# Performance work log

Measured on AMD Instinct MI355X. Metric: run time of the kernel, lower is better.

Reference implementation:

```python
import jax, jax.numpy as jnp
import numpy as np

NL, DM, DS, DC, EX = 4, 1024, 16, 4, 2
DI = EX * DM          # 2048 inner dim
DTR = DM // 16        # 64 dt_rank
HID, OUT = 2048, 1000
B, L = 2, 1024
EPS = 1e-5

def _ln(x, w, b):
    m = jnp.mean(x, -1, keepdims=True)
    v = jnp.var(x, -1, keepdims=True)
    return (x - m) / jnp.sqrt(v + EPS) * w + b

def _silu(x):
    return x * jax.nn.sigmoid(x)

def _dwconv(x, w, b):
    # x: (B,L,C), w: (C,K) depthwise causal conv
    K = w.shape[1]
    xp = jnp.pad(x, ((0, 0), (K - 1, 0), (0, 0)))
    kern = jnp.transpose(w)[:, None, :]  # (K,1,C)
    y = jax.lax.conv_general_dilated(xp, kern, (1,), 'VALID',
                                     dimension_numbers=('NLC', 'LIO', 'NLC'),
                                     feature_group_count=x.shape[-1])
    return y + b

def _selective_scan(xs_, dt, Bm, Cm, A, Dv):
    # xs_, dt: (B,L,DI); Bm, Cm: (B,L,DS); A: (DI,DS); Dv: (DI,)
    def step(h, inp):
        x_t, dt_t, B_t, C_t = inp  # (B,DI),(B,DI),(B,DS),(B,DS)
        dA = jnp.exp(dt_t[..., None] * A)                       # (B,DI,DS)
        h = dA * h + dt_t[..., None] * B_t[:, None, :] * x_t[..., None]
        return h, jnp.einsum('bdn,bn->bd', h, C_t)
    h0 = jnp.zeros((xs_.shape[0], A.shape[0], A.shape[1]), xs_.dtype)
    seq = tuple(jnp.swapaxes(t, 0, 1) for t in (xs_, dt, Bm, Cm))
    _, ys = jax.lax.scan(step, h0, seq)
    return jnp.swapaxes(ys, 0, 1) + xs_ * Dv

def _mamba_block(x, ipw, cw, cb, xpw, dpw, dpb, Alog, Dv, opw):
    xz = jnp.einsum('bld,ed->ble', x, ipw)          # (B,L,2*DI)
    xs_, z = jnp.split(xz, 2, -1)
    xs_ = _silu(_dwconv(xs_, cw, cb))
    xdbl = jnp.einsum('bld,ed->ble', xs_, xpw)      # (B,L,DTR+2*DS)
    dt, Bm, Cm = jnp.split(xdbl, [DTR, DTR + DS], -1)
    dt = jax.nn.softplus(jnp.einsum('blr,dr->bld', dt, dpw) + dpb)
    A = -jnp.exp(Alog)
    y = _selective_scan(xs_, dt, Bm, Cm, A, Dv)
    y = y * _silu(z)
    return jnp.einsum('bld,ed->ble', y, opw)

def setup_inputs() -> dict:
    key = jax.random.key(0)
    ks = jax.random.split(key, 16)
    s = 0.02
    return {
        'x': jax.random.normal(ks[0], (B, L, DM), jnp.float32),
        'ln_w': jnp.ones((NL, DM)), 'ln_b': jnp.zeros((NL, DM)),
        'in_proj_w': jax.random.normal(ks[1], (NL, 2 * DI, DM)) * s,
        'conv_w': jax.random.normal(ks[2], (NL, DI, DC)) * s,
        'conv_b': jnp.zeros((NL, DI)),
        'x_proj_w': jax.random.normal(ks[3], (NL, DTR + 2 * DS, DI)) * s,
        'dt_proj_w': jax.random.normal(ks[4], (NL, DI, DTR)) * s,
        'dt_proj_b': jax.random.uniform(ks[5], (NL, DI), minval=-4.0, maxval=-2.0),
        'A_log': jnp.log(jnp.broadcast_to(jnp.arange(1, DS + 1, dtype=jnp.float32), (NL, DI, DS)) + 0.0),
        'Dv': jnp.ones((NL, DI)),
        'out_proj_w': jax.random.normal(ks[6], (NL, DM, DI)) * s,
        'fn_w': jnp.ones((DM,)), 'fn_b': jnp.zeros((DM,)),
        'h1_w': jax.random.normal(ks[7], (HID, DM)) * s, 'h1_b': jnp.zeros((HID,)),
        'hln_w': jnp.ones((HID,)), 'hln_b': jnp.zeros((HID,)),
        'h2_w': jax.random.normal(ks[8], (OUT, HID)) * s, 'h2_b': jnp.zeros((OUT,)),
    }

def reference(x, ln_w, ln_b, in_proj_w, conv_w, conv_b, x_proj_w, dt_proj_w,
              dt_proj_b, A_log, Dv, out_proj_w, fn_w, fn_b,
              h1_w, h1_b, hln_w, hln_b, h2_w, h2_b):
    for i in range(NL):
        res = x
        xn = _ln(x, ln_w[i], ln_b[i])
        x = _mamba_block(xn, in_proj_w[i], conv_w[i], conv_b[i], x_proj_w[i],
                         dt_proj_w[i], dt_proj_b[i], A_log[i], Dv[i], out_proj_w[i]) + res
    x = _ln(x, fn_w, fn_b)
    last = x[:, -1, :]                               # (B, DM)
    h = jax.nn.gelu(_ln(last @ h1_w.T + h1_b, hln_w, hln_b), approximate=False)
    return h @ h2_w.T + h2_b                         # (B, OUT)
```

## Files before the change

### kernel.cpp

```cpp
#include <hip/hip_runtime.h>

typedef unsigned short u16;
using short8 = __attribute__((ext_vector_type(8))) short;
using f32x4  = __attribute__((ext_vector_type(4))) float;

#define NLAYER 4
#define DMODEL 1024
#define DSTATE 16
#define DINNER 2048
#define DTRANK 64
#define SEQL   1024
#define NBATCH 2
#define MTOK   2048
#define NCH    64
#define CLEN   16

__device__ __forceinline__ u16 f2bf(float f) {
  union { float f; unsigned int u; } cv; cv.f = f;
  return (u16)((cv.u + 0x7FFFu + ((cv.u >> 16) & 1u)) >> 16);
}
__device__ __forceinline__ float bf2f(u16 v) {
  union { unsigned int u; float f; } cv; cv.u = ((unsigned int)v) << 16; return cv.f;
}

__global__ __launch_bounds__(256) void f32_to_bf16_l(const float* __restrict__ src,
                                                     u16* __restrict__ dst, int nper) {
  int l = blockIdx.y;
  int i4 = (blockIdx.x * 256 + threadIdx.x) * 4;
  if (i4 >= nper) return;
  float4 v = *(const float4*)&src[(size_t)l * nper + i4];
  ushort4 o; o.x = f2bf(v.x); o.y = f2bf(v.y); o.z = f2bf(v.z); o.w = f2bf(v.w);
  *(ushort4*)&dst[(size_t)l * nper + i4] = o;
}

__global__ __launch_bounds__(256) void cvt_pad_xproj_l(const float* __restrict__ src,
                                                       u16* __restrict__ dst) {
  int l = blockIdx.y;
  int i4 = (blockIdx.x * 256 + threadIdx.x) * 4;
  int row = i4 >> 11, col = i4 & 2047;
  float4 v = make_float4(0.f, 0.f, 0.f, 0.f);
  if (row < 96) v = *(const float4*)&src[(size_t)l * 96 * 2048 + row * 2048 + col];
  ushort4 o; o.x = f2bf(v.x); o.y = f2bf(v.y); o.z = f2bf(v.z); o.w = f2bf(v.w);
  *(ushort4*)&dst[(size_t)l * 128 * 2048 + i4] = o;
}

__global__ __launch_bounds__(256) void ln_to_bf16_k(const float* __restrict__ X,
    const float* __restrict__ w, const float* __restrict__ b, u16* __restrict__ out) {
  int row = blockIdx.x, tid = threadIdx.x;
  const float* x = X + (size_t)row * 1024;
  float4 v = ((const float4*)x)[tid];
  float s = v.x + v.y + v.z + v.w;
  float q = v.x*v.x + v.y*v.y + v.z*v.z + v.w*v.w;
  for (int o = 32; o; o >>= 1) { s += __shfl_down(s, o); q += __shfl_down(q, o); }
  __shared__ float sb[4], qb[4];
  int wv = tid >> 6, lane = tid & 63;
  if (lane == 0) { sb[wv] = s; qb[wv] = q; }
  __syncthreads();
  s = sb[0] + sb[1] + sb[2] + sb[3];
  q = qb[0] + qb[1] + qb[2] + qb[3];
  float mean = s * (1.f / 1024.f);
  float var  = q * (1.f / 1024.f) - mean * mean;
  float rstd = rsqrtf(var + 1e-5f);
  float4 wv4 = ((const float4*)w)[tid];
  float4 bv4 = ((const float4*)b)[tid];
  ushort4 o4;
  o4.x = f2bf((v.x - mean) * rstd * wv4.x + bv4.x);
  o4.y = f2bf((v.y - mean) * rstd * wv4.y + bv4.y);
  o4.z = f2bf((v.z - mean) * rstd * wv4.z + bv4.z);
  o4.w = f2bf((v.w - mean) * rstd * wv4.w + bv4.w);
  ((ushort4*)(out + (size_t)row * 1024))[tid] = o4;
}

__device__ __forceinline__ void stage_tile(const u16* G, int ld, int row0, int k0,
                                           u16* S, int tid) {
  int w = tid >> 6;
#pragma unroll
  for (int j = 0; j < 2; ++j) {
    int t = tid + j * 256;
    int r = t >> 2;
    int c = (t & 3) << 3;
    const u16* g = G + (size_t)(row0 + r) * ld + (k0 + c);
    u16* s = S + w * 512 + j * 2048;
    __builtin_amdgcn_global_load_lds((const __attribute__((address_space(1))) void*)g,
                                     (__attribute__((address_space(3))) void*)s,
                                     16, 0, 0);
  }
}

template<int EPI>
__global__ __launch_bounds__(256) void gemm_bt(const u16* __restrict__ A,
    const u16* __restrict__ Bw, float* __restrict__ C,
    int lda, int ldb, int ldc, int kchunk) {
  __shared__ u16 As[2][128 * 32];
  __shared__ u16 Bs[2][128 * 32];
  int tid = threadIdx.x;
  int bm = blockIdx.x, bn = blockIdx.y;
  int kb = blockIdx.z * kchunk, ke = kb + kchunk;
  int lane = tid & 63, w = tid >> 6;
  int wr = (w >> 1) * 64, wc = (w & 1) * 64;
  int fr = lane & 15;
  int kg = (lane >> 4) * 8;
  f32x4 acc[4][4] = {};
  int cur = 0;
  stage_tile(A, lda, bm * 128, kb, As[0], tid);
  stage_tile(Bw, ldb, bn * 128, kb, Bs[0], tid);
  __syncthreads();
  for (int k0 = kb; k0 < ke; k0 += 32) {
    int kn = k0 + 32;
    if (kn < ke) {
      stage_tile(A, lda, bm * 128, kn, As[cur ^ 1], tid);
      stage_tile(Bw, ldb, bn * 128, kn, Bs[cur ^ 1], tid);
    }
    short8 a[4], b[4];
#pragma unroll
    for (int mf = 0; mf < 4; ++mf)
      a[mf] = *(const short8*)&As[cur][(wr + mf * 16 + fr) * 32 + kg];
#pragma unroll
    for (int nf = 0; nf < 4; ++nf)
      b[nf] = *(const short8*)&Bs[cur][(wc + nf * 16 + fr) * 32 + kg];
#pragma unroll
    for (int mf = 0; mf < 4; ++mf)
#pragma unroll
      for (int nf = 0; nf < 4; ++nf)
        acc[mf][nf] = __builtin_amdgcn_mfma_f32_16x16x32_bf16(a[mf], b[nf], acc[mf][nf], 0, 0, 0);
    __syncthreads();
    cur ^= 1;
  }
  int r0 = bm * 128 + wr + (lane >> 4) * 4;
  int c0 = bn * 128 + wc + fr;
#pragma unroll
  for (int mf = 0; mf < 4; ++mf) {
#pragma unroll
    for (int nf = 0; nf < 4; ++nf) {
#pragma unroll
      for (int r = 0; r < 4; ++r) {
        int gr = r0 + mf * 16 + r;
        int gc = c0 + nf * 16;
        float v = acc[mf][nf][r];
        size_t idx = (size_t)gr * ldc + gc;
        if (EPI == 1) {
          ((u16*)C)[idx] = f2bf(v);
        } else {
          atomicAdd(&C[idx], v);
        }
      }
    }
  }
}

__global__ __launch_bounds__(256) void conv_silu_k(const u16* __restrict__ xzb,
    const float* __restrict__ cw, const float* __restrict__ cb,
    u16* __restrict__ xsb) {
  int idx = blockIdx.x * 256 + threadIdx.x;
  int m = idx >> 9;
  int d = (idx & 511) << 2;
  int t = m & (SEQL - 1);
  float4 w0 = *(const float4*)&cw[(d + 0) * 4];
  float4 w1 = *(const float4*)&cw[(d + 1) * 4];
  float4 w2 = *(const float4*)&cw[(d + 2) * 4];
  float4 w3 = *(const float4*)&cw[(d + 3) * 4];
  float4 acc = *(const float4*)&cb[d];
#pragma unroll
  for (int j = 0; j < 4; ++j) {
    int tt = t - 3 + j;
    if (tt >= 0) {
      ushort4 xv = *(const ushort4*)&xzb[(size_t)(m - 3 + j) * 4096 + d];
      acc.x += bf2f(xv.x) * ((const float*)&w0)[j];
      acc.y += bf2f(xv.y) * ((const float*)&w1)[j];
      acc.z += bf2f(xv.z) * ((const float*)&w2)[j];
      acc.w += bf2f(xv.w) * ((const float*)&w3)[j];
    }
  }
  float4 o;
  o.x = acc.x / (1.f + __expf(-acc.x));
  o.y = acc.y / (1.f + __expf(-acc.y));
  o.z = acc.z / (1.f + __expf(-acc.z));
  o.w = acc.w / (1.f + __expf(-acc.w));
  ushort4 ob; ob.x = f2bf(o.x); ob.y = f2bf(o.y); ob.z = f2bf(o.z); ob.w = f2bf(o.w);
  *(ushort4*)&xsb[(size_t)m * 2048 + d] = ob;
}

__global__ __launch_bounds__(256) void gemm_dt_k(const float* __restrict__ Af,
    const u16* __restrict__ Bw, const float* __restrict__ bias, u16* __restrict__ Cout) {
  __shared__ u16 As[128 * 32];
  __shared__ u16 Bs[128 * 32];
  int tid = threadIdx.x;
  int bm = blockIdx.x, bn = blockIdx.y;
  int lane = tid & 63, w = tid >> 6;
  int wr = (w >> 1) * 64, wc = (w & 1) * 64;
  int fr = lane & 15;
  int kg = (lane >> 4) * 8;
  f32x4 acc[4][4] = {};
  int r  = tid >> 1;
  int cc = (tid & 1) * 16;
  for (int k0 = 0; k0 < 64; k0 += 32) {
    const float* src = &Af[(size_t)(bm * 128 + r) * 128 + k0 + cc];
    float4 f0 = *(const float4*)&src[0];
    float4 f1 = *(const float4*)&src[4];
    float4 f2 = *(const float4*)&src[8];
    float4 f3 = *(const float4*)&src[12];
    short8 o0, o1;
    o0[0]=(short)f2bf(f0.x); o0[1]=(short)f2bf(f0.y); o0[2]=(short)f2bf(f0.z); o0[3]=(short)f2bf(f0.w);
    o0[4]=(short)f2bf(f1.x); o0[5]=(short)f2bf(f1.y); o0[6]=(short)f2bf(f1.z); o0[7]=(short)f2bf(f1.w);
    o1[0]=(short)f2bf(f2.x); o1[1]=(short)f2bf(f2.y); o1[2]=(short)f2bf(f2.z); o1[3]=(short)f2bf(f2.w);
    o1[4]=(short)f2bf(f3.x); o1[5]=(short)f2bf(f3.y); o1[6]=(short)f2bf(f3.z); o1[7]=(short)f2bf(f3.w);
    __syncthreads();
    *(short8*)&As[r * 32 + cc]     = o0;
    *(short8*)&As[r * 32 + cc + 8] = o1;
    stage_tile(Bw, 64, bn * 128, k0, Bs, tid);
    __syncthreads();
    short8 a[4], b[4];
#pragma unroll
    for (int mf = 0; mf < 4; ++mf)
      a[mf] = *(const short8*)&As[(wr + mf * 16 + fr) * 32 + kg];
#pragma unroll
    for (int nf = 0; nf < 4; ++nf)
      b[nf] = *(const short8*)&Bs[(wc + nf * 16 + fr) * 32 + kg];
#pragma unroll
    for (int mf = 0; mf < 4; ++mf)
#pragma unroll
      for (int nf = 0; nf < 4; ++nf)
        acc[mf][nf] = __builtin_amdgcn_mfma_f32_16x16x32_bf16(a[mf], b[nf], acc[mf][nf], 0, 0, 0);
  }
  int r0 = bm * 128 + wr + (lane >> 4) * 4;
  int c0 = bn * 128 + wc + fr;
#pragma unroll
  for (int mf = 0; mf < 4; ++mf)
#pragma unroll
    for (int nf = 0; nf < 4; ++nf)
#pragma unroll
      for (int rr = 0; rr < 4; ++rr) {
        int gr = r0 + mf * 16 + rr;
        int gc = c0 + nf * 16;
        float v = acc[mf][nf][rr] + bias[gc];
        v = (v > 20.f) ? v : log1pf(__expf(v));
        Cout[(size_t)gr * 2048 + gc] = f2bf(v);
      }
}

__global__ __launch_bounds__(256) void scan_part1(const u16* __restrict__ dtb,
    const u16* __restrict__ xsb, const float* __restrict__ xdbl,
    const float* __restrict__ Alog, float* __restrict__ PS) {
  int tid = threadIdx.x;
  int dg = blockIdx.x & 7;
  int ch = (blockIdx.x >> 3) & (NCH - 1);
  int b  = blockIdx.x >> 9;
  int d  = dg * 256 + tid;
  float Ar[16];
#pragma unroll
  for (int q = 0; q < 4; ++q) {
    float4 a = *(const float4*)&Alog[d * 16 + q * 4];
    Ar[q*4+0] = -__expf(a.x); Ar[q*4+1] = -__expf(a.y);
    Ar[q*4+2] = -__expf(a.z); Ar[q*4+3] = -__expf(a.w);
  }
  __shared__ float Bsh[CLEN][16];
  {
    int t = tid >> 4, n = tid & 15;
    int mm = b * SEQL + ch * CLEN + t;
    Bsh[t][n] = xdbl[mm * 128 + 64 + n];
  }
  __syncthreads();
  int mbase = b * SEQL + ch * CLEN;
  float dtv[CLEN], xv[CLEN];
#pragma unroll
  for (int t = 0; t < CLEN; ++t) dtv[t] = bf2f(dtb[(size_t)(mbase + t) * 2048 + d]);
#pragma unroll
  for (int t = 0; t < CLEN; ++t) xv[t] = bf2f(xsb[(size_t)(mbase + t) * 2048 + d]);
  float S[16];
#pragma unroll
  for (int n = 0; n < 16; ++n) S[n] = 0.f;
  float sumdt = 0.f;
  for (int t = 0; t < CLEN; ++t) {
    sumdt += dtv[t];
    float dx = dtv[t] * xv[t];
    float4 B0 = *(const float4*)&Bsh[t][0];
    float4 B1 = *(const float4*)&Bsh[t][4];
    float4 B2 = *(const float4*)&Bsh[t][8];
    float4 B3 = *(const float4*)&Bsh[t][12];
    const float* Bp[4] = {(const float*)&B0, (const float*)&B1, (const float*)&B2, (const float*)&B3};
#pragma unroll
    for (int n = 0; n < 16; ++n)
      S[n] = __expf(dtv[t] * Ar[n]) * S[n] + dx * Bp[n >> 2][n & 3];
  }
  float* p = PS + ((size_t)(b * NCH + ch) * 2048 + d) * 32;
#pragma unroll
  for (int n = 0; n < 16; ++n) p[n] = S[n];
#pragma unroll
  for (int n = 0; n < 16; ++n) p[16 + n] = __expf(Ar[n] * sumdt);
}

__global__ __launch_bounds__(256) void scan_prefix(const float* __restrict__ PS,
                                                   float* __restrict__ Hstart) {
  int id = blockIdx.x * 256 + threadIdx.x;
  int n = id & 15;
  int d = (id >> 4) & 2047;
  int b = id >> 15;
  size_t sbase = ((size_t)b * NCH) * 2048 * 32 + (size_t)d * 32 + n;
  size_t hbase = ((size_t)b * NCH) * 2048 * 16 + (size_t)d * 16 + n;
  float h = 0.f;
#pragma unroll 8
  for (int ch = 0; ch < NCH; ++ch) {
    Hstart[hbase + (size_t)ch * (2048 * 16)] = h;
    float S = PS[sbase + (size_t)ch * (2048 * 32)];
    float P = PS[sbase + (size_t)ch * (2048 * 32) + 16];
    h = fmaf(P, h, S);
  }
}

__global__ __launch_bounds__(256) void scan_part2(const u16* __restrict__ dtb,
    const u16* __restrict__ xsb, const float* __restrict__ xdbl,
    const float* __restrict__ Alog, const float* __restrict__ Dv,
    const u16* __restrict__ xzb, const float* __restrict__ Hstart,
    u16* __restrict__ yg) {
  int tid = threadIdx.x;
  int dg = blockIdx.x & 7;
  int ch = (blockIdx.x >> 3) & (NCH - 1);
  int b  = blockIdx.x >> 9;
  int d  = dg * 256 + tid;
  float Ar[16];
#pragma unroll
  for (int q = 0; q < 4; ++q) {
    float4 a = *(const float4*)&Alog[d * 16 + q * 4];
    Ar[q*4+0] = -__expf(a.x); Ar[q*4+1] = -__expf(a.y);
    Ar[q*4+2] = -__expf(a.z); Ar[q*4+3] = -__expf(a.w);
  }
  float Dvd = Dv[d];
  __shared__ float BCs[CLEN][32];
  {
    int t = tid >> 5, n = tid & 31;
    int mm = b * SEQL + ch * CLEN + t;
    BCs[t][n] = xdbl[mm * 128 + 64 + n];
    BCs[t + 8][n] = xdbl[(mm + 8) * 128 + 64 + n];
  }
  const float* hs = Hstart + ((size_t)(b * NCH + ch) * 2048 + d) * 16;
  float h[16];
#pragma unroll
  for (int q = 0; q < 4; ++q) {
    float4 hv = *(const float4*)&hs[q * 4];
    h[q*4+0] = hv.x; h[q*4+1] = hv.y; h[q*4+2] = hv.z; h[q*4+3] = hv.w;
  }
  int mbase = b * SEQL + ch * CLEN;
  float dtv[CLEN], xv[CLEN], zv[CLEN];
#pragma unroll
  for (int t = 0; t < CLEN; ++t) dtv[t] = bf2f(dtb[(size_t)(mbase + t) * 2048 + d]);
#pragma unroll
  for (int t = 0; t < CLEN; ++t) xv[t] = bf2f(xsb[(size_t)(mbase + t) * 2048 + d]);
#pragma unroll
  for (int t = 0; t < CLEN; ++t) zv[t] = bf2f(xzb[(size_t)(mbase + t) * 4096 + 2048 + d]);
  __syncthreads();
  for (int t = 0; t < CLEN; ++t) {
    float dx = dtv[t] * xv[t];
    float4 B0 = *(const float4*)&BCs[t][0];
    float4 B1 = *(const float4*)&BCs[t][4];
    float4 B2 = *(const float4*)&BCs[t][8];
    float4 B3 = *(const float4*)&BCs[t][12];
    float4 C0 = *(const float4*)&BCs[t][16];
    float4 C1 = *(const float4*)&BCs[t][20];
    float4 C2 = *(const float4*)&BCs[t][24];
    float4 C3 = *(const float4*)&BCs[t][28];
    const float* Bp[4] = {(const float*)&B0, (const float*)&B1, (const float*)&B2, (const float*)&B3};
    const float* Cp[4] = {(const float*)&C0, (const float*)&C1, (const float*)&C2, (const float*)&C3};
#pragma unroll
    for (int n = 0; n < 16; ++n)
      h[n] = __expf(dtv[t] * Ar[n]) * h[n] + dx * Bp[n >> 2][n & 3];
    float y0 = 0.f, y1 = 0.f, y2 = 0.f, y3 = 0.f;
#pragma unroll
    for (int n = 0; n < 4; ++n) {
      y0 += h[n]      * Cp[0][n];
      y1 += h[4 + n]  * Cp[1][n];
      y2 += h[8 + n]  * Cp[2][n];
      y3 += h[12 + n] * Cp[3][n];
    }
    float y = (y0 + y1) + (y2 + y3) + xv[t] * Dvd;
    float sz = zv[t] / (1.f + __expf(-zv[t]));
    yg[(size_t)(mbase + t) * 2048 + d] = f2bf(y * sz);
  }
}

__global__ __launch_bounds__(256) void final_ln_last_k(const float* __restrict__ xb,
    const float* __restrict__ w, const float* __restrict__ b, float* __restrict__ out) {
  int bb = blockIdx.x, tid = threadIdx.x;
  const float* x = xb + (size_t)(bb * 1024 + 1023) * 1024;
  float4 v = ((const float4*)x)[tid];
  float s = v.x + v.y + v.z + v.w;
  float q = v.x*v.x + v.y*v.y + v.z*v.z + v.w*v.w;
  for (int o = 32; o; o >>= 1) { s += __shfl_down(s, o); q += __shfl_down(q, o); }
  __shared__ float sb[4], qb[4];
  int wv = tid >> 6, lane = tid & 63;
  if (lane == 0) { sb[wv] = s; qb[wv] = q; }
  __syncthreads();
  s = sb[0] + sb[1] + sb[2] + sb[3];
  q = qb[0] + qb[1] + qb[2] + qb[3];
  float mean = s * (1.f / 1024.f);
  float rstd = rsqrtf(q * (1.f / 1024.f) - mean * mean + 1e-5f);
  float4 wv4 = ((const float4*)w)[tid];
  float4 bv4 = ((const float4*)b)[tid];
  float4 o;
  o.x = (v.x - mean) * rstd * wv4.x + bv4.x;
  o.y = (v.y - mean) * rstd * wv4.y + bv4.y;
  o.z = (v.z - mean) * rstd * wv4.z + bv4.z;
  o.w = (v.w - mean) * rstd * wv4.w + bv4.w;
  ((float4*)(out + bb * 1024))[tid] = o;
}

__global__ __launch_bounds__(256) void gemv_head1_k(const float* __restrict__ X,
    const float* __restrict__ W, const float* __restrict__ bias, float* __restrict__ out) {
  int gw = (blockIdx.x * 256 + threadIdx.x) >> 6;
  int lane = threadIdx.x & 63;
  int b = gw >> 11, j = gw & 2047;
  const float* x = X + b * 1024;
  const float* w = W + (size_t)j * 1024;
  float s = 0.f;
#pragma unroll
  for (int q = 0; q < 4; ++q) {
    int col = q * 256 + lane * 4;
    float4 xv = *(const float4*)&x[col];
    float4 wv = *(const float4*)&w[col];
    s += xv.x*wv.x + xv.y*wv.y + xv.z*wv.z + xv.w*wv.w;
  }
  for (int o = 32; o; o >>= 1) s += __shfl_down(s, o);
  if (lane == 0) out[gw] = s + bias[j];
}

__global__ __launch_bounds__(256) void ln_gelu_k(const float* __restrict__ X,
    const float* __restrict__ w, const float* __restrict__ b, float* __restrict__ out) {
  int row = blockIdx.x, tid = threadIdx.x;
  const float* x = X + (size_t)row * 2048;
  float4 v0 = ((const float4*)x)[tid];
  float4 v1 = ((const float4*)x)[tid + 256];
  float s = v0.x+v0.y+v0.z+v0.w + v1.x+v1.y+v1.z+v1.w;
  float q = v0.x*v0.x+v0.y*v0.y+v0.z*v0.z+v0.w*v0.w
          + v1.x*v1.x+v1.y*v1.y+v1.z*v1.z+v1.w*v1.w;
  for (int o = 32; o; o >>= 1) { s += __shfl_down(s, o); q += __shfl_down(q, o); }
  __shared__ float sb[4], qb[4];
  int wv = tid >> 6, lane = tid & 63;
  if (lane == 0) { sb[wv] = s; qb[wv] = q; }
  __syncthreads();
  s = sb[0] + sb[1] + sb[2] + sb[3];
  q = qb[0] + qb[1] + qb[2] + qb[3];
  float mean = s * (1.f / 2048.f);
  float rstd = rsqrtf(q * (1.f / 2048.f) - mean * mean + 1e-5f);
  float* o0 = out + (size_t)row * 2048;
#pragma unroll
  for (int h = 0; h < 2; ++h) {
    float4 v = h ? v1 : v0;
    int c0 = tid * 4 + h * 1024;
    float4 wv4 = *(const float4*)&w[c0];
    float4 bv4 = *(const float4*)&b[c0];
    float4 g;
    g.x = (v.x - mean) * rstd * wv4.x + bv4.x;
    g.y = (v.y - mean) * rstd * wv4.y + bv4.y;
    g.z = (v.z - mean) * rstd * wv4.z + bv4.z;
    g.w = (v.w - mean) * rstd * wv4.w + bv4.w;
    g.x = 0.5f * g.x * (1.f + erff(g.x * 0.70710678f));
    g.y = 0.5f * g.y * (1.f + erff(g.y * 0.70710678f));
    g.z = 0.5f * g.z * (1.f + erff(g.z * 0.70710678f));
    g.w = 0.5f * g.w * (1.f + erff(g.w * 0.70710678f));
    *(float4*)&o0[c0] = g;
  }
}

__global__ __launch_bounds__(256) void gemv_head2_k(const float* __restrict__ X,
    const float* __restrict__ W, const float* __restrict__ bias, float* __restrict__ out) {
  int gw = (blockIdx.x * 256 + threadIdx.x) >> 6;
  int lane = threadIdx.x & 63;
  int b = (gw >= 1000) ? 1 : 0;
  int j = gw - b * 1000;
  const float* x = X + b * 2048;
  const float* w = W + (size_t)j * 2048;
  float s = 0.f;
#pragma unroll
  for (int q = 0; q < 8; ++q) {
    int col = q * 256 + lane * 4;
    float4 xv = *(const float4*)&x[col];
    float4 wv = *(const float4*)&w[col];
    s += xv.x*wv.x + xv.y*wv.y + xv.z*wv.z + xv.w*wv.w;
  }
  for (int o = 32; o; o >>= 1) s += __shfl_down(s, o);
  if (lane == 0) out[gw] = s + bias[j];
}

extern "C" void kernel_launch(void* const* d_in, const int* in_sizes, int n_in,
                              void* d_out, int out_size, void* d_ws, size_t ws_size,
                              hipStream_t stream) {
  const float* x_in = (const float*)d_in[0];
  const float* lnw  = (const float*)d_in[1];
  const float* lnb  = (const float*)d_in[2];
  const float* ipw  = (const float*)d_in[3];
  const float* cw   = (const float*)d_in[4];
  const float* cb   = (const float*)d_in[5];
  const float* xpw  = (const float*)d_in[6];
  const float* dpw  = (const float*)d_in[7];
  const float* dpb  = (const float*)d_in[8];
  const float* Alog = (const float*)d_in[9];
  const float* Dv   = (const float*)d_in[10];
  const float* opw  = (const float*)d_in[11];
  const float* fnw  = (const float*)d_in[12];
  const float* fnb  = (const float*)d_in[13];
  const float* h1w  = (const float*)d_in[14];
  const float* h1b  = (const float*)d_in[15];
  const float* hlnw = (const float*)d_in[16];
  const float* hlnb = (const float*)d_in[17];
  const float* h2w  = (const float*)d_in[18];
  const float* h2b  = (const float*)d_in[19];
  float* out = (float*)d_out;

  char* ws = (char*)d_ws;
  size_t off = 0;
  auto alloc = [&](size_t bytes) -> void* {
    void* p = ws + off; off += (bytes + 255) & ~(size_t)255; return p;
  };
  float* x_buf   = (float*)alloc((size_t)MTOK * DMODEL * 4);
  u16*   xn_bf   = (u16*)  alloc((size_t)MTOK * DMODEL * 2);
  u16*   xz_bf   = (u16*)  alloc((size_t)MTOK * 2 * DINNER * 2);
  u16*   xs_bf   = (u16*)  alloc((size_t)MTOK * DINNER * 2);
  float* xdbl4   = (float*)alloc((size_t)NLAYER * MTOK * 128 * 4);
  u16*   dtb     = (u16*)  alloc((size_t)MTOK * DINNER * 2);
  u16*   yg_bf   = (u16*)  alloc((size_t)MTOK * DINNER * 2);
  u16*   w_ip4   = (u16*)  alloc((size_t)NLAYER * 2 * DINNER * DMODEL * 2);
  u16*   w_xp4   = (u16*)  alloc((size_t)NLAYER * 128 * DINNER * 2);
  u16*   w_dt4   = (u16*)  alloc((size_t)NLAYER * DINNER * DTRANK * 2);
  u16*   w_op4   = (u16*)  alloc((size_t)NLAYER * DMODEL * DINNER * 2);
  float* PS      = (float*)alloc((size_t)NBATCH * NCH * DINNER * 32 * 4);
  float* Hstart  = (float*)alloc((size_t)NBATCH * NCH * DINNER * 16 * 4);
  float* lastn   = (float*)alloc(2 * 1024 * 4);
  float* hpre    = (float*)alloc(2 * 2048 * 4);
  float* hbuf    = (float*)alloc(2 * 2048 * 4);

  hipMemcpyAsync(x_buf, x_in, (size_t)MTOK * DMODEL * 4, hipMemcpyDeviceToDevice, stream);
  { dim3 g(4096, 4); f32_to_bf16_l<<<g, 256, 0, stream>>>(ipw, w_ip4, 2 * DINNER * DMODEL); }
  { dim3 g(256, 4);  cvt_pad_xproj_l<<<g, 256, 0, stream>>>(xpw, w_xp4); }
  { dim3 g(128, 4);  f32_to_bf16_l<<<g, 256, 0, stream>>>(dpw, w_dt4, DINNER * DTRANK); }
  { dim3 g(2048, 4); f32_to_bf16_l<<<g, 256, 0, stream>>>(opw, w_op4, DMODEL * DINNER); }
  hipMemsetAsync(xdbl4, 0, (size_t)NLAYER * MTOK * 128 * 4, stream);

  for (int i = 0; i < NLAYER; ++i) {
    float* xdbl_l = xdbl4 + (size_t)i * MTOK * 128;
    ln_to_bf16_k<<<MTOK, 256, 0, stream>>>(x_buf, lnw + i * DMODEL, lnb + i * DMODEL, xn_bf);
    { dim3 g(16, 32, 1);
      gemm_bt<1><<<g, 256, 0, stream>>>(xn_bf, w_ip4 + (size_t)i * 2 * DINNER * DMODEL,
                                        (float*)xz_bf, 1024, 1024, 4096, 1024); }
    conv_silu_k<<<4096, 256, 0, stream>>>(xz_bf, cw + (size_t)i * DINNER * 4, cb + i * DINNER, xs_bf);
    { dim3 g(16, 1, 8);
      gemm_bt<3><<<g, 256, 0, stream>>>(xs_bf, w_xp4 + (size_t)i * 128 * DINNER,
                                        xdbl_l, 2048, 2048, 128, 256); }
    { dim3 g(16, 16, 1);
      gemm_dt_k<<<g, 256, 0, stream>>>(xdbl_l, w_dt4 + (size_t)i * DINNER * DTRANK,
                                       dpb + i * DINNER, dtb); }
    scan_part1<<<1024, 256, 0, stream>>>(dtb, xs_bf, xdbl_l, Alog + (size_t)i * DINNER * DSTATE, PS);
    scan_prefix<<<256, 256, 0, stream>>>(PS, Hstart);
    scan_part2<<<1024, 256, 0, stream>>>(dtb, xs_bf, xdbl_l, Alog + (size_t)i * DINNER * DSTATE,
                                         Dv + i * DINNER, xz_bf, Hstart, yg_bf);
    { dim3 g(16, 8, 2);
      gemm_bt<3><<<g, 256, 0, stream>>>(yg_bf, w_op4 + (size_t)i * DMODEL * DINNER,
                                        x_buf, 2048, 2048, 1024, 1024); }
  }
  final_ln_last_k<<<2, 256, 0, stream>>>(x_buf, fnw, fnb, lastn);
  gemv_head1_k<<<1024, 256, 0, stream>>>(lastn, h1w, h1b, hpre);
  ln_gelu_k<<<2, 256, 0, stream>>>(hpre, hlnw, hlnb, hbuf);
  gemv_head2_k<<<500, 256, 0, stream>>>(hbuf, h2w, h2b, out);
  (void)in_sizes; (void)n_in; (void)out_size; (void)ws_size;
}
```

Baseline: 736.2 us.

## Vectorize conv, shrink scan intermediates to bf16, fuse head LN+GEMV kernels

The depthwise conv+SiLU kernel now processes 8 channels per thread with 16-byte loads and stores. The chunked scan no longer writes per-chunk decay products: scan_prefix recomputes exp(A*sumdt) from a per-chunk sumdt array. Chunk start states are stored as bf16 in an n-major layout, cutting scan traffic at some cost in state precision. The x_proj split-K GEMM uses twice as many K splits, and the final LN, GEMV, LN and GELU head kernels are fused into two launches, with each block redundantly recomputing the normalization.

```diff
diff --git a/kernel.cpp b/kernel.cpp
--- a/kernel.cpp
+++ b/kernel.cpp
@@ -152,32 +152,35 @@
     const float* __restrict__ cw, const float* __restrict__ cb,
     u16* __restrict__ xsb) {
   int idx = blockIdx.x * 256 + threadIdx.x;
-  int m = idx >> 9;
-  int d = (idx & 511) << 2;
+  int m = idx >> 8;
+  int d = (idx & 255) << 3;
   int t = m & (SEQL - 1);
-  float4 w0 = *(const float4*)&cw[(d + 0) * 4];
-  float4 w1 = *(const float4*)&cw[(d + 1) * 4];
-  float4 w2 = *(const float4*)&cw[(d + 2) * 4];
-  float4 w3 = *(const float4*)&cw[(d + 3) * 4];
-  float4 acc = *(const float4*)&cb[d];
+  float4 w4[8];
+#pragma unroll
+  for (int i = 0; i < 8; ++i) w4[i] = *(const float4*)&cw[(d + i) * 4];
+  float acc[8];
+#pragma unroll
+  for (int q = 0; q < 2; ++q) {
+    float4 c4 = *(const float4*)&cb[d + q * 4];
+    acc[q*4+0] = c4.x; acc[q*4+1] = c4.y; acc[q*4+2] = c4.z; acc[q*4+3] = c4.w;
+  }
 #pragma unroll
   for (int j = 0; j < 4; ++j) {
     int tt = t - 3 + j;
     if (tt >= 0) {
-      ushort4 xv = *(const ushort4*)&xzb[(size_t)(m - 3 + j) * 4096 + d];
-      acc.x += bf2f(xv.x) * ((const float*)&w0)[j];
-      acc.y += bf2f(xv.y) * ((const float*)&w1)[j];
-      acc.z += bf2f(xv.z) * ((const float*)&w2)[j];
-      acc.w += bf2f(xv.w) * ((const float*)&w3)[j];
+      short8 xv = *(const short8*)&xzb[(size_t)(m - 3 + j) * 4096 + d];
+#pragma unroll
+      for (int i = 0; i < 8; ++i)
+        acc[i] += bf2f((u16)xv[i]) * ((const float*)&w4[i])[j];
     }
   }
-  float4 o;
-  o.x = acc.x / (1.f + __expf(-acc.x));
-  o.y = acc.y / (1.f + __expf(-acc.y));
-  o.z = acc.z / (1.f + __expf(-acc.z));
-  o.w = acc.w / (1.f + __expf(-acc.w));
-  ushort4 ob; ob.x = f2bf(o.x); ob.y = f2bf(o.y); ob.z = f2bf(o.z); ob.w = f2bf(o.w);
-  *(ushort4*)&xsb[(size_t)m * 2048 + d] = ob;
+  short8 ob;
+#pragma unroll
+  for (int i = 0; i < 8; ++i) {
+    float o = acc[i] / (1.f + __expf(-acc[i]));
+    ob[i] = (short)f2bf(o);
+  }
+  *(short8*)&xsb[(size_t)m * 2048 + d] = ob;
 }
 
 __global__ __launch_bounds__(256) void gemm_dt_k(const float* __restrict__ Af,
@@ -240,7 +243,7 @@
 
 __global__ __launch_bounds__(256) void scan_part1(const u16* __restrict__ dtb,
     const u16* __restrict__ xsb, const float* __restrict__ xdbl,
-    const float* __restrict__ Alog, float* __restrict__ PS) {
+    const float* __restrict__ Alog, float* __restrict__ PS_S, float* __restrict__ sumdt_a) {
   int tid = threadIdx.x;
   int dg = blockIdx.x & 7;
   int ch = (blockIdx.x >> 3) & (NCH - 1);
@@ -282,35 +285,36 @@
     for (int n = 0; n < 16; ++n)
       S[n] = __expf(dtv[t] * Ar[n]) * S[n] + dx * Bp[n >> 2][n & 3];
   }
-  float* p = PS + ((size_t)(b * NCH + ch) * 2048 + d) * 32;
-#pragma unroll
-  for (int n = 0; n < 16; ++n) p[n] = S[n];
-#pragma unroll
-  for (int n = 0; n < 16; ++n) p[16 + n] = __expf(Ar[n] * sumdt);
-}
-
-__global__ __launch_bounds__(256) void scan_prefix(const float* __restrict__ PS,
-                                                   float* __restrict__ Hstart) {
+  size_t base = ((size_t)(b * NCH + ch) * 16) * 2048 + d;
+#pragma unroll
+  for (int n = 0; n < 16; ++n) PS_S[base + (size_t)n * 2048] = S[n];
+  sumdt_a[(size_t)(b * NCH + ch) * 2048 + d] = sumdt;
+}
+
+__global__ __launch_bounds__(256) void scan_prefix(const float* __restrict__ PS_S,
+    const float* __restrict__ sumdt_a, const float* __restrict__ Alog,
+    u16* __restrict__ Hb) {
   int id = blockIdx.x * 256 + threadIdx.x;
-  int n = id & 15;
-  int d = (id >> 4) & 2047;
+  int d = id & 2047;
+  int n = (id >> 11) & 15;
   int b = id >> 15;
-  size_t sbase = ((size_t)b * NCH) * 2048 * 32 + (size_t)d * 32 + n;
-  size_t hbase = ((size_t)b * NCH) * 2048 * 16 + (size_t)d * 16 + n;
+  float Ar = -__expf(Alog[d * 16 + n]);
+  size_t sbase = ((size_t)(b * NCH) * 16 + n) * 2048 + d;
+  size_t dbase = (size_t)(b * NCH) * 2048 + d;
   float h = 0.f;
 #pragma unroll 8
   for (int ch = 0; ch < NCH; ++ch) {
-    Hstart[hbase + (size_t)ch * (2048 * 16)] = h;
-    float S = PS[sbase + (size_t)ch * (2048 * 32)];
-    float P = PS[sbase + (size_t)ch * (2048 * 32) + 16];
-    h = fmaf(P, h, S);
+    Hb[sbase + (size_t)ch * (16 * 2048)] = f2bf(h);
+    float S  = PS_S[sbase + (size_t)ch * (16 * 2048)];
+    float sd = sumdt_a[dbase + (size_t)ch * 2048];
+    h = fmaf(__expf(Ar * sd), h, S);
   }
 }
 
 __global__ __launch_bounds__(256) void scan_part2(const u16* __restrict__ dtb,
     const u16* __restrict__ xsb, const float* __restrict__ xdbl,
     const float* __restrict__ Alog, const float* __restrict__ Dv,
-    const u16* __restrict__ xzb, const float* __restrict__ Hstart,
+    const u16* __restrict__ xzb, const u16* __restrict__ Hb,
     u16* __restrict__ yg) {
   int tid = threadIdx.x;
   int dg = blockIdx.x & 7;
@@ -332,13 +336,10 @@
     BCs[t][n] = xdbl[mm * 128 + 64 + n];
     BCs[t + 8][n] = xdbl[(mm + 8) * 128 + 64 + n];
   }
-  const float* hs = Hstart + ((size_t)(b * NCH + ch) * 2048 + d) * 16;
+  size_t hbase = ((size_t)(b * NCH + ch) * 16) * 2048 + d;
   float h[16];
 #pragma unroll
-  for (int q = 0; q < 4; ++q) {
-    float4 hv = *(const float4*)&hs[q * 4];
-    h[q*4+0] = hv.x; h[q*4+1] = hv.y; h[q*4+2] = hv.z; h[q*4+3] = hv.w;
-  }
+  for (int n = 0; n < 16; ++n) h[n] = bf2f(Hb[hbase + (size_t)n * 2048]);
   int mbase = b * SEQL + ch * CLEN;
   float dtv[CLEN], xv[CLEN], zv[CLEN];
 #pragma unroll
@@ -377,55 +378,59 @@
   }
 }
 
-__global__ __launch_bounds__(256) void final_ln_last_k(const float* __restrict__ xb,
-    const float* __restrict__ w, const float* __restrict__ b, float* __restrict__ out) {
-  int bb = blockIdx.x, tid = threadIdx.x;
-  const float* x = xb + (size_t)(bb * 1024 + 1023) * 1024;
+__global__ __launch_bounds__(256) void lnlast_gemv1_k(const float* __restrict__ xb,
+    const float* __restrict__ fnw, const float* __restrict__ fnb,
+    const float* __restrict__ h1w, const float* __restrict__ h1b,
+    float* __restrict__ hpre) {
+  int blk = blockIdx.x, tid = threadIdx.x;
+  int b = blk >> 9;
+  int jbase = (blk & 511) * 4;
+  int wv = tid >> 6, lane = tid & 63;
+  const float* x = xb + (size_t)(b * 1024 + 1023) * 1024;
   float4 v = ((const float4*)x)[tid];
   float s = v.x + v.y + v.z + v.w;
   float q = v.x*v.x + v.y*v.y + v.z*v.z + v.w*v.w;
   for (int o = 32; o; o >>= 1) { s += __shfl_down(s, o); q += __shfl_down(q, o); }
   __shared__ float sb[4], qb[4];
-  int wv = tid >> 6, lane = tid & 63;
+  __shared__ float row[1024];
   if (lane == 0) { sb[wv] = s; qb[wv] = q; }
   __syncthreads();
   s = sb[0] + sb[1] + sb[2] + sb[3];
   q = qb[0] + qb[1] + qb[2] + qb[3];
   float mean = s * (1.f / 1024.f);
   float rstd = rsqrtf(q * (1.f / 1024.f) - mean * mean + 1e-5f);
-  float4 wv4 = ((const float4*)w)[tid];
-  float4 bv4 = ((const float4*)b)[tid];
+  float4 wv4 = ((const float4*)fnw)[tid];
+  float4 bv4 = ((const float4*)fnb)[tid];
   float4 o;
   o.x = (v.x - mean) * rstd * wv4.x + bv4.x;
   o.y = (v.y - mean) * rstd * wv4.y + bv4.y;
   o.z = (v.z - mean) * rstd * wv4.z + bv4.z;
   o.w = (v.w - mean) * rstd * wv4.w + bv4.w;
-  ((float4*)(out + bb * 1024))[tid] = o;
-}
-
-__global__ __launch_bounds__(256) void gemv_head1_k(const float* __restrict__ X,
-    const float* __restrict__ W, const float* __restrict__ bias, float* __restrict__ out) {
-  int gw = (blockIdx.x * 256 + threadIdx.x) >> 6;
-  int lane = threadIdx.x & 63;
-  int b = gw >> 11, j = gw & 2047;
-  const float* x = X + b * 1024;
-  const float* w = W + (size_t)j * 1024;
-  float s = 0.f;
-#pragma unroll
-  for (int q = 0; q < 4; ++q) {
-    int col = q * 256 + lane * 4;
-    float4 xv = *(const float4*)&x[col];
-    float4 wv = *(const float4*)&w[col];
-    s += xv.x*wv.x + xv.y*wv.y + xv.z*wv.z + xv.w*wv.w;
-  }
-  for (int o = 32; o; o >>= 1) s += __shfl_down(s, o);
-  if (lane == 0) out[gw] = s + bias[j];
-}
-
-__global__ __launch_bounds__(256) void ln_gelu_k(const float* __restrict__ X,
-    const float* __restrict__ w, const float* __restrict__ b, float* __restrict__ out) {
-  int row = blockIdx.x, tid = threadIdx.x;
-  const float* x = X + (size_t)row * 2048;
+  ((float4*)row)[tid] = o;
+  __syncthreads();
+  int j = jbase + wv;
+  const float* w = h1w + (size_t)j * 1024;
+  float acc = 0.f;
+#pragma unroll
+  for (int qq = 0; qq < 4; ++qq) {
+    int col = qq * 256 + lane * 4;
+    float4 xv = *(const float4*)&row[col];
+    float4 wvv = *(const float4*)&w[col];
+    acc += xv.x*wvv.x + xv.y*wvv.y + xv.z*wvv.z + xv.w*wvv.w;
+  }
+  for (int o2 = 32; o2; o2 >>= 1) acc += __shfl_down(acc, o2);
+  if (lane == 0) hpre[b * 2048 + j] = acc + h1b[j];
+}
+
+__global__ __launch_bounds__(256) void lngelu_gemv2_k(const float* __restrict__ hpre,
+    const float* __restrict__ hlnw, const float* __restrict__ hlnb,
+    const float* __restrict__ h2w, const float* __restrict__ h2b,
+    float* __restrict__ out) {
+  int blk = blockIdx.x, tid = threadIdx.x;
+  int b = (blk >= 250) ? 1 : 0;
+  int jbase = (blk - b * 250) * 4;
+  int wv = tid >> 6, lane = tid & 63;
+  const float* x = hpre + b * 2048;
   float4 v0 = ((const float4*)x)[tid];
   float4 v1 = ((const float4*)x)[tid + 256];
   float s = v0.x+v0.y+v0.z+v0.w + v1.x+v1.y+v1.z+v1.w;
@@ -433,20 +438,19 @@
           + v1.x*v1.x+v1.y*v1.y+v1.z*v1.z+v1.w*v1.w;
   for (int o = 32; o; o >>= 1) { s += __shfl_down(s, o); q += __shfl_down(q, o); }
   __shared__ float sb[4], qb[4];
-  int wv = tid >> 6, lane = tid & 63;
+  __shared__ float row[2048];
   if (lane == 0) { sb[wv] = s; qb[wv] = q; }
   __syncthreads();
   s = sb[0] + sb[1] + sb[2] + sb[3];
   q = qb[0] + qb[1] + qb[2] + qb[3];
   float mean = s * (1.f / 2048.f);
   float rstd = rsqrtf(q * (1.f / 2048.f) - mean * mean + 1e-5f);
-  float* o0 = out + (size_t)row * 2048;
 #pragma unroll
   for (int h = 0; h < 2; ++h) {
     float4 v = h ? v1 : v0;
     int c0 = tid * 4 + h * 1024;
-    float4 wv4 = *(const float4*)&w[c0];
-    float4 bv4 = *(const float4*)&b[c0];
+    float4 wv4 = *(const float4*)&hlnw[c0];
+    float4 bv4 = *(const float4*)&hlnb[c0];
     float4 g;
     g.x = (v.x - mean) * rstd * wv4.x + bv4.x;
     g.y = (v.y - mean) * rstd * wv4.y + bv4.y;
@@ -456,28 +460,21 @@
     g.y = 0.5f * g.y * (1.f + erff(g.y * 0.70710678f));
     g.z = 0.5f * g.z * (1.f + erff(g.z * 0.70710678f));
     g.w = 0.5f * g.w * (1.f + erff(g.w * 0.70710678f));
-    *(float4*)&o0[c0] = g;
-  }
-}
-
-__global__ __launch_bounds__(256) void gemv_head2_k(const float* __restrict__ X,
-    const float* __restrict__ W, const float* __restrict__ bias, float* __restrict__ out) {
-  int gw = (blockIdx.x * 256 + threadIdx.x) >> 6;
-  int lane = threadIdx.x & 63;
-  int b = (gw >= 1000) ? 1 : 0;
-  int j = gw - b * 1000;
-  const float* x = X + b * 2048;
-  const float* w = W + (size_t)j * 2048;
-  float s = 0.f;
-#pragma unroll
-  for (int q = 0; q < 8; ++q) {
-    int col = q * 256 + lane * 4;
-    float4 xv = *(const float4*)&x[col];
-    float4 wv = *(const float4*)&w[col];
-    s += xv.x*wv.x + xv.y*wv.y + xv.z*wv.z + xv.w*wv.w;
-  }
-  for (int o = 32; o; o >>= 1) s += __shfl_down(s, o);
-  if (lane == 0) out[gw] = s + bias[j];
+    *(float4*)&row[c0] = g;
+  }
+  __syncthreads();
+  int j = jbase + wv;
+  const float* w = h2w + (size_t)j * 2048;
+  float acc = 0.f;
+#pragma unroll
+  for (int qq = 0; qq < 8; ++qq) {
+    int col = qq * 256 + lane * 4;
+    float4 xv = *(const float4*)&row[col];
+    float4 wvv = *(const float4*)&w[col];
+    acc += xv.x*wvv.x + xv.y*wvv.y + xv.z*wvv.z + xv.w*wvv.w;
+  }
+  for (int o2 = 32; o2; o2 >>= 1) acc += __shfl_down(acc, o2);
+  if (lane == 0) out[b * 1000 + j] = acc + h2b[j];
 }
 
 extern "C" void kernel_launch(void* const* d_in, const int* in_sizes, int n_in,
@@ -521,11 +518,10 @@
   u16*   w_xp4   = (u16*)  alloc((size_t)NLAYER * 128 * DINNER * 2);
   u16*   w_dt4   = (u16*)  alloc((size_t)NLAYER * DINNER * DTRANK * 2);
   u16*   w_op4   = (u16*)  alloc((size_t)NLAYER * DMODEL * DINNER * 2);
-  float* PS      = (float*)alloc((size_t)NBATCH * NCH * DINNER * 32 * 4);
-  float* Hstart  = (float*)alloc((size_t)NBATCH * NCH * DINNER * 16 * 4);
-  float* lastn   = (float*)alloc(2 * 1024 * 4);
+  float* PS_S    = (float*)alloc((size_t)NBATCH * NCH * 16 * 2048 * 4);
+  float* sumdt_a = (float*)alloc((size_t)NBATCH * NCH * 2048 * 4);
+  u16*   Hb      = (u16*)  alloc((size_t)NBATCH * NCH * 16 * 2048 * 2);
   float* hpre    = (float*)alloc(2 * 2048 * 4);
-  float* hbuf    = (float*)alloc(2 * 2048 * 4);
 
   hipMemcpyAsync(x_buf, x_in, (size_t)MTOK * DMODEL * 4, hipMemcpyDeviceToDevice, stream);
   { dim3 g(4096, 4); f32_to_bf16_l<<<g, 256, 0, stream>>>(ipw, w_ip4, 2 * DINNER * DMODEL); }
@@ -540,24 +536,23 @@
     { dim3 g(16, 32, 1);
       gemm_bt<1><<<g, 256, 0, stream>>>(xn_bf, w_ip4 + (size_t)i * 2 * DINNER * DMODEL,
                                         (float*)xz_bf, 1024, 1024, 4096, 1024); }
-    conv_silu_k<<<4096, 256, 0, stream>>>(xz_bf, cw + (size_t)i * DINNER * 4, cb + i * DINNER, xs_bf);
-    { dim3 g(16, 1, 8);
+    conv_silu_k<<<2048, 256, 0, stream>>>(xz_bf, cw + (size_t)i * DINNER * 4, cb + i * DINNER, xs_bf);
+    { dim3 g(16, 1, 16);
       gemm_bt<3><<<g, 256, 0, stream>>>(xs_bf, w_xp4 + (size_t)i * 128 * DINNER,
-                                        xdbl_l, 2048, 2048, 128, 256); }
+                                        xdbl_l, 2048, 2048, 128, 128); }
     { dim3 g(16, 16, 1);
       gemm_dt_k<<<g, 256, 0, stream>>>(xdbl_l, w_dt4 + (size_t)i * DINNER * DTRANK,
                                        dpb + i * DINNER, dtb); }
-    scan_part1<<<1024, 256, 0, stream>>>(dtb, xs_bf, xdbl_l, Alog + (size_t)i * DINNER * DSTATE, PS);
-    scan_prefix<<<256, 256, 0, stream>>>(PS, Hstart);
+    scan_part1<<<1024, 256, 0, stream>>>(dtb, xs_bf, xdbl_l,
+                                         Alog + (size_t)i * DINNER * DSTATE, PS_S, sumdt_a);
+    scan_prefix<<<256, 256, 0, stream>>>(PS_S, sumdt_a, Alog + (size_t)i * DINNER * DSTATE, Hb);
     scan_part2<<<1024, 256, 0, stream>>>(dtb, xs_bf, xdbl_l, Alog + (size_t)i * DINNER * DSTATE,
-                                         Dv + i * DINNER, xz_bf, Hstart, yg_bf);
+                                         Dv + i * DINNER, xz_bf, Hb, yg_bf);
     { dim3 g(16, 8, 2);
       gemm_bt<3><<<g, 256, 0, stream>>>(yg_bf, w_op4 + (size_t)i * DMODEL * DINNER,
                                         x_buf, 2048, 2048, 1024, 1024); }
   }
-  final_ln_last_k<<<2, 256, 0, stream>>>(x_buf, fnw, fnb, lastn);
-  gemv_head1_k<<<1024, 256, 0, stream>>>(lastn, h1w, h1b, hpre);
-  ln_gelu_k<<<2, 256, 0, stream>>>(hpre, hlnw, hlnb, hbuf);
-  gemv_head2_k<<<500, 256, 0, stream>>>(hbuf, h2w, h2b, out);
+  lnlast_gemv1_k<<<1024, 256, 0, stream>>>(x_buf, fnw, fnb, h1w, h1b, hpre);
+  lngelu_gemv2_k<<<500, 256, 0, stream>>>(hpre, hlnw, hlnb, h2w, h2b, out);
   (void)in_sizes; (void)n_in; (void)out_size; (void)ws_size;
 }
```

Measured after the change: 745.2 us. About the same (+1.2%).
